# Optimization experiments

Measured on AMD Instinct MI355X. Metric: run time of the kernel, lower is better.

The kernel has to match this reference:

```python
import jax, jax.numpy as jnp
import numpy as np

LAMBDA_COORD = 5.0
LAMBDA_NOOBJ = 0.5
NUM_CLASSES = 20

B, S, M = 16384, 7, 16  # batch, grid size, max gt boxes per image


def _iou(a, b):
    """IoU of center-format boxes (x, y, w, h); last dim = 4."""
    ax1, ay1 = a[..., 0] - a[..., 2] / 2, a[..., 1] - a[..., 3] / 2
    ax2, ay2 = a[..., 0] + a[..., 2] / 2, a[..., 1] + a[..., 3] / 2
    bx1, by1 = b[..., 0] - b[..., 2] / 2, b[..., 1] - b[..., 3] / 2
    bx2, by2 = b[..., 0] + b[..., 2] / 2, b[..., 1] + b[..., 3] / 2
    iw = jnp.clip(jnp.minimum(ax2, bx2) - jnp.maximum(ax1, bx1), 0.0)
    ih = jnp.clip(jnp.minimum(ay2, by2) - jnp.maximum(ay1, by1), 0.0)
    inter = iw * ih
    union = a[..., 2] * a[..., 3] + b[..., 2] * b[..., 3] - inter
    return inter / (union + 1e-6)


def setup_inputs() -> dict:
    key = jax.random.key(0)
    k1, k2, k3 = jax.random.split(key, 3)
    pred = jax.random.normal(k1, (B, S, S, 30), dtype=jnp.float32)
    gt_xywh = jax.random.uniform(k2, (B, M, 4), dtype=jnp.float32)
    gt_class = jax.random.randint(k3, (B, M), 0, NUM_CLASSES, dtype=jnp.int32)
    return {"pred": pred, "gt_xywh": gt_xywh, "gt_class": gt_class}


def reference(pred, gt_xywh, gt_class):
    b, s = pred.shape[0], pred.shape[1]
    m = gt_xywh.shape[1]
    gx, gy, gw, gh = (gt_xywh[..., i] for i in range(4))

    # NOTE: original code computes row from x and col from y (kept faithfully).
    rows = jnp.clip(jnp.floor(gx * s).astype(jnp.int32), 0, s - 1)
    cols = jnp.clip(jnp.floor(gy * s).astype(jnp.int32), 0, s - 1)
    cell = rows * s + cols                      # [B, M]

    bidx = jnp.arange(b)[:, None]               # [B, 1]
    midx = jnp.broadcast_to(jnp.arange(m, dtype=jnp.int32), (b, m))

    # first-occurrence-per-cell dedup == the sequential `cells_with_obj` skip
    first = jnp.full((b, s * s), m, jnp.int32).at[bidx, cell].min(midx)
    keep = (midx == first[bidx, cell]).astype(pred.dtype)  # [B, M]

    # cell-relative target (x uses col, y uses row, as in the original)
    tgt = jnp.stack([gx * s - cols, gy * s - rows,
                     jnp.sqrt(gw), jnp.sqrt(gh)], axis=-1)   # [B, M, 4]

    cp = pred[bidx, rows, cols]                 # [B, M, 30]

    iou1 = _iou(cp[..., 0:4], tgt)
    iou2 = _iou(cp[..., 5:9], tgt)
    use2 = iou2 >= iou1                          # ties -> second box, as in torch code
    sel_box = jnp.where(use2[..., None], cp[..., 5:9], cp[..., 0:4])
    sel_conf = jnp.where(use2, cp[..., 9], cp[..., 4])
    sel_iou = jnp.where(use2, iou2, iou1)

    coord = LAMBDA_COORD * jnp.sum(keep * jnp.sum((sel_box - tgt) ** 2, axis=-1))
    # torch.tensor(pred_bbox_iou) detaches the confidence target
    conf = jnp.sum(keep * (sel_conf - jax.lax.stop_gradient(sel_iou)) ** 2)
    onehot = jax.nn.one_hot(gt_class, NUM_CLASSES, dtype=pred.dtype)
    cls = jnp.sum(keep * jnp.sum((cp[..., -NUM_CLASSES:] - onehot) ** 2, axis=-1))

    # no-object confidence term: zero out both confidences at object cells
    obj = jnp.zeros((b, s * s), bool).at[bidx, cell].set(True)   # [B, S*S]
    conf_pred = pred[..., jnp.array([4, 9])].reshape(b, s * s, 2)
    noobj = LAMBDA_NOOBJ * jnp.sum(jnp.where(obj[..., None], 0.0, conf_pred) ** 2)

    return (coord + conf + cls + noobj) / b
```

## Files before the change

kernel.cpp:

```cpp
#include <hip/hip_runtime.h>
#include <math.h>

#define B_TOT 16384
#define S_    7
#define M_    16
#define C_    30
#define NC_   20
#define CELLS (S_*S_)
#define PER_B (CELLS*C_)
#define GPB   8
#define BLK   256
#define NBLK  (B_TOT/GPB)

__device__ __forceinline__ float iou_cf(float ax,float ay,float aw,float ah,
                                        float bx,float by,float bw,float bh){
  float ax1=ax-aw*0.5f, ay1=ay-ah*0.5f, ax2=ax+aw*0.5f, ay2=ay+ah*0.5f;
  float bx1=bx-bw*0.5f, by1=by-bh*0.5f, bx2=bx+bw*0.5f, by2=by+bh*0.5f;
  float iw=fmaxf(fminf(ax2,bx2)-fmaxf(ax1,bx1), 0.f);
  float ih=fmaxf(fminf(ay2,by2)-fmaxf(ay1,by1), 0.f);
  float inter=iw*ih;
  float uni=aw*ah+bw*bh-inter;
  return inter/(uni+1e-6f);
}

__global__ __launch_bounds__(BLK) void yolo_main(const float* __restrict__ pred,
                                                 const float* __restrict__ gt_xywh,
                                                 const int*   __restrict__ gt_class,
                                                 float*       __restrict__ partial)
{
  const int t   = threadIdx.x;
  const int blk = blockIdx.x;
  const int base_b = blk * GPB;

  int   cell = 0, cls = 0;
  bool  keep = false;
  float tx=0.f, ty=0.f, tw=0.f, th=0.f;
  const int lb = t >> 4;
  const int m  = t & 15;
  if (t < GPB*M_) {
    float4 g = ((const float4*)gt_xywh)[base_b*M_ + t];
    int row = (int)floorf(g.x * (float)S_); row = min(max(row,0), S_-1);
    int col = (int)floorf(g.y * (float)S_); col = min(max(col,0), S_-1);
    cell = row*S_ + col;
    tx = g.x*(float)S_ - (float)col;
    ty = g.y*(float)S_ - (float)row;
    tw = sqrtf(g.z);
    th = sqrtf(g.w);
    cls  = gt_class[base_b*M_ + t];
    keep = true;
    #pragma unroll
    for (int j = 0; j < M_; ++j) {
      int cj = __shfl(cell, j, M_);
      if (j < m && cj == cell) keep = false;
    }
  }

  float accn = 0.f;
  const float4* s4 = (const float4*)(pred + (size_t)base_b * PER_B);
  const int n4 = GPB*PER_B/4;
  int c0 = (t*4) % 30;
  for (int i = t; i < n4; i += BLK) {
    float4 v = s4[i];
    float vv[4] = {v.x, v.y, v.z, v.w};
    #pragma unroll
    for (int k = 0; k < 4; ++k) {
      int c = c0 + k; if (c >= 30) c -= 30;
      if (c == 4 || c == 9) accn += vv[k]*vv[k];
    }
    c0 += 4; if (c0 >= 30) c0 -= 30;
  }

  float accb = 0.f;
  if (keep) {
    const float* cp = pred + (size_t)(base_b + lb) * PER_B + cell*C_;
    float p0=cp[0],p1=cp[1],p2=cp[2],p3=cp[3],p4=cp[4];
    float p5=cp[5],p6=cp[6],p7=cp[7],p8=cp[8],p9=cp[9];
    float i1 = iou_cf(p0,p1,p2,p3, tx,ty,tw,th);
    float i2 = iou_cf(p5,p6,p7,p8, tx,ty,tw,th);
    bool  u2 = (i2 >= i1);
    float sx = u2?p5:p0, sy = u2?p6:p1, sw = u2?p7:p2, sh = u2?p8:p3;
    float sc = u2?p9:p4, si = u2?i2:i1;
    float dx=sx-tx, dy=sy-ty, dw=sw-tw, dh=sh-th;
    accb += 5.0f*(dx*dx + dy*dy + dw*dw + dh*dh);
    float dc = sc - si;
    accb += dc*dc;
    #pragma unroll
    for (int c = 0; c < NC_; ++c) {
      float d = cp[10+c] - ((c==cls) ? 1.f : 0.f);
      accb += d*d;
    }
    accb -= 0.5f*(p4*p4 + p9*p9);
  }

  float acc = accb + 0.5f*accn;

  #pragma unroll
  for (int off = 32; off > 0; off >>= 1) acc += __shfl_down(acc, off);
  __shared__ float wsum[BLK/64];
  if ((t & 63) == 0) wsum[t >> 6] = acc;
  __syncthreads();
  if (t == 0) partial[blk] = wsum[0] + wsum[1] + wsum[2] + wsum[3];
}

__global__ __launch_bounds__(256) void yolo_reduce(const float* __restrict__ partial,
                                                   float* __restrict__ out)
{
  const int t = threadIdx.x;
  float a = 0.f;
  for (int i = t; i < NBLK; i += 256) a += partial[i];
  #pragma unroll
  for (int off = 32; off > 0; off >>= 1) a += __shfl_down(a, off);
  __shared__ float wsum[4];
  if ((t & 63) == 0) wsum[t >> 6] = a;
  __syncthreads();
  if (t == 0) out[0] = (wsum[0] + wsum[1] + wsum[2] + wsum[3]) * (1.0f/(float)B_TOT);
}

extern "C" void kernel_launch(void* const* d_in, const int* in_sizes, int n_in,
                              void* d_out, int out_size, void* d_ws, size_t ws_size,
                              hipStream_t stream) {
  const float* pred     = (const float*)d_in[0];
  const float* gt_xywh  = (const float*)d_in[1];
  const int*   gt_class = (const int*)d_in[2];
  float* partial = (float*)d_ws;
  yolo_main<<<NBLK, BLK, 0, stream>>>(pred, gt_xywh, gt_class, partial);
  yolo_reduce<<<1, 256, 0, stream>>>(partial, (float*)d_out);
}
```

Measured before the change: 153.0 us.

## Fuse final reduction via atomicAdd and process 16 images per block

Doubles the images handled per block so all 256 threads own one ground-truth box, removing the idle half of threads in the box phase. Drops the separate reduce kernel by having each block atomically add its scaled partial sum into the output after a memset. This saves one kernel launch and the partial-buffer round trip, but halves the block count and adds a memset plus atomic contention. The floating-point summation order now varies from run to run.

```diff
diff --git a/kernel.cpp b/kernel.cpp
--- a/kernel.cpp
+++ b/kernel.cpp
@@ -8,7 +8,7 @@
 #define NC_   20
 #define CELLS (S_*S_)
 #define PER_B (CELLS*C_)
-#define GPB   8
+#define GPB   16
 #define BLK   256
 #define NBLK  (B_TOT/GPB)
 
@@ -23,36 +23,31 @@
   return inter/(uni+1e-6f);
 }
 
-__global__ __launch_bounds__(BLK) void yolo_main(const float* __restrict__ pred,
-                                                 const float* __restrict__ gt_xywh,
-                                                 const int*   __restrict__ gt_class,
-                                                 float*       __restrict__ partial)
+__global__ __launch_bounds__(BLK) void yolo_fused(const float* __restrict__ pred,
+                                                  const float* __restrict__ gt_xywh,
+                                                  const int*   __restrict__ gt_class,
+                                                  float*       __restrict__ out)
 {
   const int t   = threadIdx.x;
   const int blk = blockIdx.x;
   const int base_b = blk * GPB;
 
-  int   cell = 0, cls = 0;
-  bool  keep = false;
-  float tx=0.f, ty=0.f, tw=0.f, th=0.f;
   const int lb = t >> 4;
   const int m  = t & 15;
-  if (t < GPB*M_) {
-    float4 g = ((const float4*)gt_xywh)[base_b*M_ + t];
-    int row = (int)floorf(g.x * (float)S_); row = min(max(row,0), S_-1);
-    int col = (int)floorf(g.y * (float)S_); col = min(max(col,0), S_-1);
-    cell = row*S_ + col;
-    tx = g.x*(float)S_ - (float)col;
-    ty = g.y*(float)S_ - (float)row;
-    tw = sqrtf(g.z);
-    th = sqrtf(g.w);
-    cls  = gt_class[base_b*M_ + t];
-    keep = true;
-    #pragma unroll
-    for (int j = 0; j < M_; ++j) {
-      int cj = __shfl(cell, j, M_);
-      if (j < m && cj == cell) keep = false;
-    }
+  float4 g = ((const float4*)gt_xywh)[blk*BLK + t];
+  int row = (int)floorf(g.x * (float)S_); row = min(max(row,0), S_-1);
+  int col = (int)floorf(g.y * (float)S_); col = min(max(col,0), S_-1);
+  const int cell = row*S_ + col;
+  const float tx = g.x*(float)S_ - (float)col;
+  const float ty = g.y*(float)S_ - (float)row;
+  const float tw = sqrtf(g.z);
+  const float th = sqrtf(g.w);
+  const int cls  = gt_class[blk*BLK + t];
+  bool keep = true;
+  #pragma unroll
+  for (int j = 0; j < M_; ++j) {
+    int cj = __shfl(cell, j, M_);
+    if (j < m && cj == cell) keep = false;
   }
 
   float accn = 0.f;
@@ -99,21 +94,10 @@
   __shared__ float wsum[BLK/64];
   if ((t & 63) == 0) wsum[t >> 6] = acc;
   __syncthreads();
-  if (t == 0) partial[blk] = wsum[0] + wsum[1] + wsum[2] + wsum[3];
-}
-
-__global__ __launch_bounds__(256) void yolo_reduce(const float* __restrict__ partial,
-                                                   float* __restrict__ out)
-{
-  const int t = threadIdx.x;
-  float a = 0.f;
-  for (int i = t; i < NBLK; i += 256) a += partial[i];
-  #pragma unroll
-  for (int off = 32; off > 0; off >>= 1) a += __shfl_down(a, off);
-  __shared__ float wsum[4];
-  if ((t & 63) == 0) wsum[t >> 6] = a;
-  __syncthreads();
-  if (t == 0) out[0] = (wsum[0] + wsum[1] + wsum[2] + wsum[3]) * (1.0f/(float)B_TOT);
+  if (t == 0) {
+    float v = (wsum[0] + wsum[1] + wsum[2] + wsum[3]) * (1.0f/(float)B_TOT);
+    atomicAdd(out, v);
+  }
 }
 
 extern "C" void kernel_launch(void* const* d_in, const int* in_sizes, int n_in,
@@ -122,7 +106,7 @@
   const float* pred     = (const float*)d_in[0];
   const float* gt_xywh  = (const float*)d_in[1];
   const int*   gt_class = (const int*)d_in[2];
-  float* partial = (float*)d_ws;
-  yolo_main<<<NBLK, BLK, 0, stream>>>(pred, gt_xywh, gt_class, partial);
-  yolo_reduce<<<1, 256, 0, stream>>>(partial, (float*)d_out);
+  (void)d_ws; (void)ws_size;
+  hipMemsetAsync(d_out, 0, sizeof(float), stream);
+  yolo_fused<<<NBLK, BLK, 0, stream>>>(pred, gt_xywh, gt_class, (float*)d_out);
 }
```

Measured after the change: 158.3 us. 3.5% more time.
